# Kernel optimization log

Measured on AMD Instinct MI355X. Metric: run time of the kernel, lower is better.

Reference implementation:

```python
import jax, jax.numpy as jnp
import numpy as np

DIM = 3072
HEADS = 24
HEAD_DIM = 128
MLP_HIDDEN = 12288
SEQ = 2048
BATCH = 1
EPS = 1e-6


def setup_inputs() -> dict:
    key = jax.random.key(0)
    ks = jax.random.split(key, 12)
    s = 0.02
    return {
        "hidden_states": jax.random.normal(ks[0], (BATCH, SEQ, DIM), jnp.float32),
        "temb": jax.random.normal(ks[1], (BATCH, DIM), jnp.float32),
        "rope_cos": jax.random.uniform(ks[2], (SEQ, HEAD_DIM), jnp.float32),
        "rope_sin": jax.random.uniform(ks[3], (SEQ, HEAD_DIM), jnp.float32),
        # AdaLN-Zero single: Linear(dim -> 3*dim)
        "norm_w": jax.random.normal(ks[4], (3 * DIM, DIM), jnp.float32) * s,
        "norm_b": jnp.zeros((3 * DIM,), jnp.float32),
        # fused QKV + MLP projection: Linear(dim -> 3*dim + mlp_hidden)
        "qkv_mlp_w": jax.random.normal(ks[5], (3 * DIM + MLP_HIDDEN, DIM), jnp.float32) * s,
        "qkv_mlp_b": jnp.zeros((3 * DIM + MLP_HIDDEN,), jnp.float32),
        # proj_out: Linear(dim + mlp_hidden -> dim)
        "proj_w": jax.random.normal(ks[6], (DIM, DIM + MLP_HIDDEN), jnp.float32) * s,
        "proj_b": jnp.zeros((DIM,), jnp.float32),
        # qk RMSNorm weights (per head_dim)
        "rms_q_w": jnp.ones((HEAD_DIM,), jnp.float32),
        "rms_k_w": jnp.ones((HEAD_DIM,), jnp.float32),
    }


def _rms_norm(x, w):
    # x: [B,S,H,D], normalize over D
    var = jnp.mean(jnp.square(x), axis=-1, keepdims=True)
    return x * jax.lax.rsqrt(var + EPS) * w


def _apply_rope(x, cos, sin):
    # x: [B,S,H,D]; cos/sin: [S,D]. diffusers use_real, unbind_dim=-1 convention.
    xr = x.reshape(*x.shape[:-1], HEAD_DIM // 2, 2)
    rot = jnp.stack([-xr[..., 1], xr[..., 0]], axis=-1).reshape(x.shape)
    c = cos[None, :, None, :]
    s = sin[None, :, None, :]
    return x * c + rot * s


def reference(hidden_states, temb, rope_cos, rope_sin, norm_w, norm_b,
              qkv_mlp_w, qkv_mlp_b, proj_w, proj_b, rms_q_w, rms_k_w):
    B, S, _ = hidden_states.shape
    residual = hidden_states

    # --- AdaLayerNormZeroSingle ---
    mod = jax.nn.silu(temb) @ norm_w.T + norm_b          # [B, 3*dim]
    shift, scale, gate = jnp.split(mod, 3, axis=-1)       # each [B, dim]
    mu = jnp.mean(hidden_states, axis=-1, keepdims=True)
    var = jnp.mean(jnp.square(hidden_states - mu), axis=-1, keepdims=True)
    ln = (hidden_states - mu) * jax.lax.rsqrt(var + EPS)
    norm_h = ln * (1.0 + scale[:, None, :]) + shift[:, None, :]

    # --- fused QKV + MLP GEMM ---
    qkv_mlp = norm_h @ qkv_mlp_w.T + qkv_mlp_b             # [B,S,3*dim+mlp]
    qkv, mlp_h = jnp.split(qkv_mlp, [3 * DIM], axis=-1)
    mlp_out = jax.nn.gelu(mlp_h, approximate=True)         # tanh GELU

    q, k, v = jnp.split(qkv, 3, axis=-1)
    q = q.reshape(B, S, HEADS, HEAD_DIM)
    k = k.reshape(B, S, HEADS, HEAD_DIM)
    v = v.reshape(B, S, HEADS, HEAD_DIM)

    # qk RMSNorm + RoPE
    q = _apply_rope(_rms_norm(q, rms_q_w), rope_cos, rope_sin)
    k = _apply_rope(_rms_norm(k, rms_k_w), rope_cos, rope_sin)

    # scaled dot-product attention
    scale_f = 1.0 / np.sqrt(HEAD_DIM)
    scores = jnp.einsum("bqhd,bkhd->bhqk", q, k) * scale_f
    probs = jax.nn.softmax(scores, axis=-1)
    attn = jnp.einsum("bhqk,bkhd->bqhd", probs, v).reshape(B, S, DIM)

    # proj_out on concat(attn, gelu(mlp)) + gated residual
    cat = jnp.concatenate([attn, mlp_out], axis=-1)        # [B,S,dim+mlp]
    proj = cat @ proj_w.T + proj_b                          # [B,S,dim]
    return gate[:, None, :] * proj + residual
```

## Files before the change

### kernel.cpp

```cpp
#include <hip/hip_runtime.h>
#include <stdint.h>

typedef __bf16 bf16;
typedef __bf16 bf16x8 __attribute__((ext_vector_type(8)));
typedef __bf16 bf16x4 __attribute__((ext_vector_type(4)));
typedef float f32x4 __attribute__((ext_vector_type(4)));

#define DIM   3072
#define SEQ   2048
#define QKVW  9216
#define MLPH  12288
#define FUSED 21504
#define CATW  15360
#define HD    128
#define NH    24

__device__ __forceinline__ void gload_lds16(const void* g, void* l) {
  __builtin_amdgcn_global_load_lds((__attribute__((address_space(1))) void*)g,
                                   (__attribute__((address_space(3))) void*)l,
                                   16, 0, 0);
}

__global__ __launch_bounds__(256) void k_mod_gemv(
    const float* __restrict__ temb, const float* __restrict__ nw,
    const float* __restrict__ nb, float* __restrict__ mod)
{
  int j = blockIdx.x * 4 + (threadIdx.x >> 6);
  int lane = threadIdx.x & 63;
  const float* row = nw + (size_t)j * DIM;
  float acc = 0.f;
  #pragma unroll
  for (int k0 = 0; k0 < DIM; k0 += 256) {
    int k = k0 + lane * 4;
    float4 w = *(const float4*)(row + k);
    float4 t = *(const float4*)(temb + k);
    float s0 = t.x / (1.f + __expf(-t.x));
    float s1 = t.y / (1.f + __expf(-t.y));
    float s2 = t.z / (1.f + __expf(-t.z));
    float s3 = t.w / (1.f + __expf(-t.w));
    acc += w.x * s0 + w.y * s1 + w.z * s2 + w.w * s3;
  }
  #pragma unroll
  for (int m = 32; m >= 1; m >>= 1) acc += __shfl_xor(acc, m, 64);
  if (lane == 0) mod[j] = acc + nb[j];
}

__global__ __launch_bounds__(256) void k_ln_mod(
    const float* __restrict__ hs, const float* __restrict__ mod,
    bf16* __restrict__ nh)
{
  int m = blockIdx.x;
  int t = threadIdx.x;
  const float* x = hs + (size_t)m * DIM;
  float4 v[3];
  float s = 0.f, ss = 0.f;
  #pragma unroll
  for (int i = 0; i < 3; i++) {
    v[i] = *(const float4*)(x + i * 1024 + t * 4);
    s  += v[i].x + v[i].y + v[i].z + v[i].w;
    ss += v[i].x * v[i].x + v[i].y * v[i].y + v[i].z * v[i].z + v[i].w * v[i].w;
  }
  #pragma unroll
  for (int msk = 32; msk >= 1; msk >>= 1) {
    s  += __shfl_xor(s, msk, 64);
    ss += __shfl_xor(ss, msk, 64);
  }
  __shared__ float red[8];
  int wave = t >> 6;
  if ((t & 63) == 0) { red[wave] = s; red[4 + wave] = ss; }
  __syncthreads();
  s  = red[0] + red[1] + red[2] + red[3];
  ss = red[4] + red[5] + red[6] + red[7];
  float mu  = s * (1.f / DIM);
  float var = ss * (1.f / DIM) - mu * mu;
  float rstd = rsqrtf(var + 1e-6f);
  #pragma unroll
  for (int i = 0; i < 3; i++) {
    int col = i * 1024 + t * 4;
    const float* sc = mod + DIM + col;
    const float* sh = mod + col;
    float4 vv = v[i];
    bf16x4 o;
    o[0] = (bf16)((vv.x - mu) * rstd * (1.f + sc[0]) + sh[0]);
    o[1] = (bf16)((vv.y - mu) * rstd * (1.f + sc[1]) + sh[1]);
    o[2] = (bf16)((vv.z - mu) * rstd * (1.f + sc[2]) + sh[2]);
    o[3] = (bf16)((vv.w - mu) * rstd * (1.f + sc[3]) + sh[3]);
    *(bf16x4*)(nh + (size_t)m * DIM + col) = o;
  }
}

__global__ __launch_bounds__(256) void k_cvt(
    const float* __restrict__ s, bf16* __restrict__ d, size_t n)
{
  size_t stride = (size_t)gridDim.x * 256 * 8;
  for (size_t i = ((size_t)blockIdx.x * 256 + threadIdx.x) * 8; i < n; i += stride) {
    float4 a = *(const float4*)(s + i);
    float4 b = *(const float4*)(s + i + 4);
    bf16x8 h;
    h[0] = (bf16)a.x; h[1] = (bf16)a.y; h[2] = (bf16)a.z; h[3] = (bf16)a.w;
    h[4] = (bf16)b.x; h[5] = (bf16)b.y; h[6] = (bf16)b.z; h[7] = (bf16)b.w;
    *(bf16x8*)(d + i) = h;
  }
}

#define MFMA_B16(a, b, c) __builtin_amdgcn_mfma_f32_16x16x32_bf16(a, b, c, 0, 0, 0)

template<int MODE>
__global__ __launch_bounds__(512, 2) void k_gemm8(
    const bf16* __restrict__ A, const bf16* __restrict__ B,
    const float* __restrict__ bias, int K, int ntn, int nkp,
    bf16* __restrict__ oq, bf16* __restrict__ ocat, float* __restrict__ pk)
{
  __shared__ bf16 lds[65536];
  int tid = threadIdx.x;
  int wave = tid >> 6, lane = tid & 63;
  int wm = wave >> 2, wn = wave & 3;

  int nwg = gridDim.x;
  int bid = blockIdx.x;
  int swz = (bid & 7) * (nwg >> 3) + (bid >> 3);
  int mt = swz & 7;
  int rest = swz >> 3;
  int nt = rest % ntn;
  int kc = rest / ntn;
  int m0 = mt * 256, n0 = nt * 256;
  int Kp = K / nkp;
  int kbeg = kc * Kp;
  int NT = Kp >> 6;

  const bf16* Ag = A + (size_t)m0 * K + kbeg;
  const bf16* Bg = B + (size_t)n0 * K + kbeg;

  auto stA = [&](int kt, int q) {
    int kw = kt >= NT ? kt - NT : kt;
    #pragma unroll
    for (int j = 0; j < 2; j++) {
      int c = j * 16 + q * 8 + wave;
      gload_lds16(Ag + (size_t)((c >> 1) * 16 + (lane & 15)) * K
                     + ((c & 1) * 32 + (lane >> 4) * 8) + kw * 64,
                  &lds[((kt & 1) << 15) + c * 512]);
    }
  };
  auto stB = [&](int kt, int q) {
    int kw = kt >= NT ? kt - NT : kt;
    #pragma unroll
    for (int j = 0; j < 2; j++) {
      int v = j * 8 + wave;
      int c = (v >> 2) * 8 + q * 4 + (v & 3);
      gload_lds16(Bg + (size_t)((c >> 1) * 16 + (lane & 15)) * K
                     + ((c & 1) * 32 + (lane >> 4) * 8) + kw * 64,
                  &lds[((kt & 1) << 15) + 16384 + c * 512]);
    }
  };

  f32x4 acc[8][4];
  #pragma unroll
  for (int i = 0; i < 8; i++)
    #pragma unroll
    for (int j = 0; j < 4; j++) acc[i][j] = (f32x4){0.f, 0.f, 0.f, 0.f};

  const int abase = wm * 8192;
  const int bbase = 16384 + wn * 4096;
  const int lo = lane * 8;
  bf16x8 af[8][2], bfr[4][2];

  #define RD_A(MI0, BO) \
    _Pragma("unroll") for (int mi = 0; mi < 4; mi++) \
    _Pragma("unroll") for (int ks = 0; ks < 2; ks++) \
      af[MI0 + mi][ks] = *(const bf16x8*)&lds[(BO) + abase + ((MI0 + mi) * 2 + ks) * 512 + lo];
  #define RD_B(NI0, BO) \
    _Pragma("unroll") for (int ni = 0; ni < 2; ni++) \
    _Pragma("unroll") for (int ks = 0; ks < 2; ks++) \
      bfr[NI0 + ni][ks] = *(const bf16x8*)&lds[(BO) + bbase + ((NI0 + ni) * 2 + ks) * 512 + lo];
  #define QUAD(MI0, NI0) \
    __builtin_amdgcn_s_setprio(1); \
    _Pragma("unroll") for (int mi = 0; mi < 4; mi++) \
    _Pragma("unroll") for (int ni = 0; ni < 2; ni++) \
    _Pragma("unroll") for (int ks = 0; ks < 2; ks++) \
      acc[MI0 + mi][NI0 + ni] = MFMA_B16(af[MI0 + mi][ks], bfr[NI0 + ni][ks], acc[MI0 + mi][NI0 + ni]); \
    __builtin_amdgcn_s_setprio(0);
  #define BAR()   __builtin_amdgcn_s_barrier()
  #define LGKM0() asm volatile("s_waitcnt lgkmcnt(0)" ::: "memory")
  #define LGKM8() asm volatile("s_waitcnt lgkmcnt(8)" ::: "memory")
  #define VM6()   asm volatile("s_waitcnt vmcnt(6)" ::: "memory")
  #define SB0()   __builtin_amdgcn_sched_barrier(0)

  stA(0, 0); stB(0, 0); stA(0, 1); stB(0, 1);
  stA(1, 0); stB(1, 0); stA(1, 1);
  VM6();
  BAR();

  for (int it = 0; it < NT; it += 2) {
    int ta = it, tb = it + 1;
    RD_A(0, 0) RD_B(0, 0)
    stB(tb, 1);
    LGKM8();
    BAR(); LGKM0(); SB0();
    QUAD(0, 0)
    BAR();
    RD_A(4, 0)
    stA(ta + 2, 0);
    BAR(); LGKM0(); SB0();
    QUAD(4, 0)
    BAR();
    RD_B(2, 0)
    stB(ta + 2, 0);
    BAR(); LGKM0(); SB0();
    QUAD(0, 2)
    BAR();
    stA(ta + 2, 1);
    VM6();
    BAR(); SB0();
    QUAD(4, 2)
    BAR();
    RD_A(0, 32768) RD_B(0, 32768)
    stB(ta + 2, 1);
    LGKM8();
    BAR(); LGKM0(); SB0();
    QUAD(0, 0)
    BAR();
    RD_A(4, 32768)
    stA(tb + 2, 0);
    BAR(); LGKM0(); SB0();
    QUAD(4, 0)
    BAR();
    RD_B(2, 32768)
    stB(tb + 2, 0);
    BAR(); LGKM0(); SB0();
    QUAD(0, 2)
    BAR();
    stA(tb + 2, 1);
    VM6();
    BAR(); SB0();
    QUAD(4, 2)
    BAR();
  }

  int rr = (lane >> 4) * 4, cl = lane & 15;
  int mw0 = m0 + wm * 128, nw0 = n0 + wn * 64;
  #pragma unroll
  for (int mi = 0; mi < 8; mi++) {
    #pragma unroll
    for (int ni = 0; ni < 4; ni++) {
      int n = nw0 + ni * 16 + cl;
      #pragma unroll
      for (int r = 0; r < 4; r++) {
        int m = mw0 + mi * 16 + rr + r;
        float v = acc[mi][ni][r];
        if (MODE == 0) {
          v += bias[n];
          if (n < QKVW) {
            oq[(size_t)m * QKVW + n] = (bf16)v;
          } else {
            float g = 0.5f * v * (1.f + tanhf(0.7978845608028654f * (v + 0.044715f * v * v * v)));
            ocat[(size_t)m * CATW + DIM + (n - QKVW)] = (bf16)g;
          }
        } else {
          pk[(size_t)kc * SEQ * DIM + (size_t)m * DIM + n] = v;
        }
      }
    }
  }
}

template<int MODE>
__global__ __launch_bounds__(256) void k_gemm2(
    const bf16* __restrict__ A, const float* __restrict__ Bf,
    const float* __restrict__ bias, int K, int ntn,
    bf16* __restrict__ oq, bf16* __restrict__ ocat,
    const float* __restrict__ gate, const float* __restrict__ resid,
    float* __restrict__ of)
{
  __shared__ bf16 sA[8192];
  __shared__ bf16 sB[8192];
  int nwg = gridDim.x;
  int bid = blockIdx.x;
  int swz = (bid & 7) * (nwg >> 3) + (bid >> 3);
  int mt = swz & 15, nt = swz >> 4;
  int m0 = mt * 128, n0 = nt * 128;
  int tid = threadIdx.x;
  int wave = tid >> 6, lane = tid & 63;
  int wr = wave >> 1, wc = wave & 1;

  size_t aoff[4], boff[4];
  bf16* la[4];
  bf16* lb[4];
  #pragma unroll
  for (int i = 0; i < 4; i++) {
    int c = wave * 4 + i;
    int rt = c >> 1, kt = c & 1;
    int row = rt * 16 + (lane & 15);
    int col = kt * 32 + (lane >> 4) * 8;
    aoff[i] = (size_t)(m0 + row) * K + col;
    boff[i] = (size_t)(n0 + row) * K + col;
    la[i] = sA + c * 512;
    lb[i] = sB + c * 512;
  }
  f32x4 acc[4][4];
  #pragma unroll
  for (int i = 0; i < 4; i++)
    #pragma unroll
    for (int j = 0; j < 4; j++) acc[i][j] = (f32x4){0.f, 0.f, 0.f, 0.f};

  for (int kk = 0; kk < K; kk += 64) {
    #pragma unroll
    for (int i = 0; i < 4; i++)
      gload_lds16(A + aoff[i] + kk, la[i]);
    #pragma unroll
    for (int i = 0; i < 4; i++) {
      const float* g = Bf + boff[i] + kk;
      float4 f0 = *(const float4*)g;
      float4 f1 = *(const float4*)(g + 4);
      bf16x8 h;
      h[0] = (bf16)f0.x; h[1] = (bf16)f0.y; h[2] = (bf16)f0.z; h[3] = (bf16)f0.w;
      h[4] = (bf16)f1.x; h[5] = (bf16)f1.y; h[6] = (bf16)f1.z; h[7] = (bf16)f1.w;
      *(bf16x8*)(lb[i] + lane * 8) = h;
    }
    __syncthreads();
    #pragma unroll
    for (int ks = 0; ks < 2; ks++) {
      bf16x8 af[4], bfr[4];
      #pragma unroll
      for (int mi = 0; mi < 4; mi++)
        af[mi] = *(const bf16x8*)(sA + ((wr * 4 + mi) * 2 + ks) * 512 + lane * 8);
      #pragma unroll
      for (int nj = 0; nj < 4; nj++)
        bfr[nj] = *(const bf16x8*)(sB + ((wc * 4 + nj) * 2 + ks) * 512 + lane * 8);
      #pragma unroll
      for (int mi = 0; mi < 4; mi++)
        #pragma unroll
        for (int nj = 0; nj < 4; nj++)
          acc[mi][nj] = __builtin_amdgcn_mfma_f32_16x16x32_bf16(af[mi], bfr[nj], acc[mi][nj], 0, 0, 0);
    }
    __syncthreads();
  }

  int rr = (lane >> 4) * 4;
  int cl = lane & 15;
  #pragma unroll
  for (int mi = 0; mi < 4; mi++) {
    #pragma unroll
    for (int nj = 0; nj < 4; nj++) {
      int mbase = m0 + wr * 64 + mi * 16 + rr;
      int n = n0 + wc * 64 + nj * 16 + cl;
      #pragma unroll
      for (int r = 0; r < 4; r++) {
        int m = mbase + r;
        float v = acc[mi][nj][r] + bias[n];
        if (MODE == 0) {
          if (n < QKVW) {
            oq[(size_t)m * QKVW + n] = (bf16)v;
          } else {
            float g = 0.5f * v * (1.f + tanhf(0.7978845608028654f * (v + 0.044715f * v * v * v)));
            ocat[(size_t)m * CATW + DIM + (n - QKVW)] = (bf16)g;
          }
        } else {
          of[(size_t)m * DIM + n] = gate[n] * v + resid[(size_t)m * DIM + n];
        }
      }
    }
  }
}

__global__ __launch_bounds__(256) void k_red(
    const float* __restrict__ pk, const float* __restrict__ bias,
    const float* __restrict__ gate, const float* __restrict__ resid,
    float* __restrict__ out)
{
  int m = blockIdx.x / 3;
  int n = (blockIdx.x % 3) * 1024 + threadIdx.x * 4;
  size_t idx = (size_t)m * DIM + n;
  f32x4 p0 = *(const f32x4*)(pk + idx);
  f32x4 p1 = *(const f32x4*)(pk + (size_t)SEQ * DIM + idx);
  f32x4 b  = *(const f32x4*)(bias + n);
  f32x4 g  = *(const f32x4*)(gate + n);
  f32x4 r  = *(const f32x4*)(resid + idx);
  f32x4 o;
  #pragma unroll
  for (int i = 0; i < 4; i++) o[i] = g[i] * (p0[i] + p1[i] + b[i]) + r[i];
  *(f32x4*)(out + idx) = o;
}

__global__ __launch_bounds__(256) void k_rmsrope(
    bf16* __restrict__ qkv, const float* __restrict__ rc, const float* __restrict__ rs,
    const float* __restrict__ qw, const float* __restrict__ kw)
{
  int srow = blockIdx.x >> 1;
  int isk  = blockIdx.x & 1;
  int off  = isk ? DIM : 0;
  const float* w = isk ? kw : qw;
  int g = threadIdx.x >> 5, gl = threadIdx.x & 31;
  int d = gl * 4;
  #pragma unroll
  for (int hh = 0; hh < 3; hh++) {
    int h = g + hh * 8;
    bf16* p = qkv + (size_t)srow * QKVW + off + h * HD + d;
    bf16x4 u = *(const bf16x4*)p;
    float x0 = (float)u[0], x1 = (float)u[1], x2 = (float)u[2], x3 = (float)u[3];
    float ssq = x0 * x0 + x1 * x1 + x2 * x2 + x3 * x3;
    #pragma unroll
    for (int msk = 16; msk >= 1; msk >>= 1) ssq += __shfl_xor(ssq, msk, 32);
    float r = rsqrtf(ssq * (1.f / HD) + 1e-6f);
    float y0 = x0 * r * w[d], y1 = x1 * r * w[d + 1];
    float y2 = x2 * r * w[d + 2], y3 = x3 * r * w[d + 3];
    const float* c = rc + srow * HD + d;
    const float* sn = rs + srow * HD + d;
    bf16x4 o;
    o[0] = (bf16)(y0 * c[0] - y1 * sn[0]);
    o[1] = (bf16)(y1 * c[1] + y0 * sn[1]);
    o[2] = (bf16)(y2 * c[2] - y3 * sn[2]);
    o[3] = (bf16)(y3 * c[3] + y2 * sn[3]);
    *(bf16x4*)p = o;
  }
}

__global__ __launch_bounds__(256) void k_attn(
    const bf16* __restrict__ qkv, bf16* __restrict__ cat)
{
  int h  = blockIdx.y;
  int q0 = blockIdx.x * 64;
  int tid = threadIdx.x, wave = tid >> 6, lane = tid & 63;
  int r16 = lane & 15, g4 = lane >> 4;
  __shared__ bf16 sK[32 * 136];
  __shared__ bf16 sVt[128 * 40];
  __shared__ bf16 sP[4][16 * 40];

  bf16x8 qf[4];
  {
    int qrow = q0 + wave * 16 + r16;
    const bf16* qp = qkv + (size_t)qrow * QKVW + h * HD + g4 * 8;
    #pragma unroll
    for (int kc = 0; kc < 4; kc++) qf[kc] = *(const bf16x8*)(qp + kc * 32);
  }
  f32x4 oacc[8];
  #pragma unroll
  for (int dc = 0; dc < 8; dc++) oacc[dc] = (f32x4){0.f, 0.f, 0.f, 0.f};
  float mrow[4] = {-1e30f, -1e30f, -1e30f, -1e30f};
  float lrow[4] = {0.f, 0.f, 0.f, 0.f};
  const float scale = 0.08838834764831845f;

  for (int kv0 = 0; kv0 < SEQ; kv0 += 32) {
    {
      int row = tid >> 3, c0 = (tid & 7) * 16;
      const bf16* kp = qkv + (size_t)(kv0 + row) * QKVW + DIM + h * HD + c0;
      uint4 a = *(const uint4*)kp;
      uint4 b = *(const uint4*)(kp + 8);
      *(uint4*)&sK[row * 136 + c0]     = a;
      *(uint4*)&sK[row * 136 + c0 + 8] = b;
    }
    {
      int kv = tid >> 3, c0 = (tid & 7) * 16;
      const bf16* vp = qkv + (size_t)(kv0 + kv) * QKVW + 2 * DIM + h * HD + c0;
      #pragma unroll
      for (int i = 0; i < 4; i++) {
        bf16x4 u = *(const bf16x4*)(vp + i * 4);
        sVt[(c0 + i * 4 + 0) * 40 + kv] = u[0];
        sVt[(c0 + i * 4 + 1) * 40 + kv] = u[1];
        sVt[(c0 + i * 4 + 2) * 40 + kv] = u[2];
        sVt[(c0 + i * 4 + 3) * 40 + kv] = u[3];
      }
    }
    __syncthreads();

    f32x4 sv[2];
    sv[0] = (f32x4){0.f, 0.f, 0.f, 0.f};
    sv[1] = (f32x4){0.f, 0.f, 0.f, 0.f};
    #pragma unroll
    for (int ct = 0; ct < 2; ct++)
      #pragma unroll
      for (int kc = 0; kc < 4; kc++) {
        bf16x8 kf = *(const bf16x8*)&sK[(ct * 16 + r16) * 136 + kc * 32 + g4 * 8];
        sv[ct] = __builtin_amdgcn_mfma_f32_16x16x32_bf16(qf[kc], kf, sv[ct], 0, 0, 0);
      }

    bf16* sPw = &sP[wave][0];
    #pragma unroll
    for (int r = 0; r < 4; r++) {
      float a0 = sv[0][r] * scale, a1 = sv[1][r] * scale;
      float mx = fmaxf(a0, a1);
      #pragma unroll
      for (int msk = 8; msk >= 1; msk >>= 1) mx = fmaxf(mx, __shfl_xor(mx, msk, 16));
      float mnew = fmaxf(mrow[r], mx);
      float so = __expf(mrow[r] - mnew);
      float p0 = __expf(a0 - mnew), p1 = __expf(a1 - mnew);
      float rsum = p0 + p1;
      #pragma unroll
      for (int msk = 8; msk >= 1; msk >>= 1) rsum += __shfl_xor(rsum, msk, 16);
      lrow[r] = lrow[r] * so + rsum;
      mrow[r] = mnew;
      #pragma unroll
      for (int dc = 0; dc < 8; dc++) oacc[dc][r] *= so;
      int prow = g4 * 4 + r;
      sPw[prow * 40 + r16]      = (bf16)p0;
      sPw[prow * 40 + 16 + r16] = (bf16)p1;
    }
    asm volatile("s_waitcnt lgkmcnt(0)" ::: "memory");
    __builtin_amdgcn_sched_barrier(0);
    bf16x8 pa = *(const bf16x8*)&sPw[r16 * 40 + g4 * 8];
    #pragma unroll
    for (int dc = 0; dc < 8; dc++) {
      bf16x8 vf = *(const bf16x8*)&sVt[(dc * 16 + r16) * 40 + g4 * 8];
      oacc[dc] = __builtin_amdgcn_mfma_f32_16x16x32_bf16(pa, vf, oacc[dc], 0, 0, 0);
    }
    __syncthreads();
  }

  #pragma unroll
  for (int dc = 0; dc < 8; dc++) {
    #pragma unroll
    for (int r = 0; r < 4; r++) {
      int qrow = q0 + wave * 16 + g4 * 4 + r;
      int col  = h * HD + dc * 16 + r16;
      cat[(size_t)qrow * CATW + col] = (bf16)(oacc[dc][r] / lrow[r]);
    }
  }
}

extern "C" void kernel_launch(void* const* d_in, const int* in_sizes, int n_in,
                              void* d_out, int out_size, void* d_ws, size_t ws_size,
                              hipStream_t stream) {
  const float* hs      = (const float*)d_in[0];
  const float* temb    = (const float*)d_in[1];
  const float* rope_c  = (const float*)d_in[2];
  const float* rope_s  = (const float*)d_in[3];
  const float* norm_w  = (const float*)d_in[4];
  const float* norm_b  = (const float*)d_in[5];
  const float* qkvml_w = (const float*)d_in[6];
  const float* qkvml_b = (const float*)d_in[7];
  const float* proj_w  = (const float*)d_in[8];
  const float* proj_b  = (const float*)d_in[9];
  const float* rms_q_w = (const float*)d_in[10];
  const float* rms_k_w = (const float*)d_in[11];
  float* out = (float*)d_out;

  char* ws = (char*)d_ws;
  size_t off = 0;
  float* mod  = (float*)(ws + off); off += 40960;
  bf16*  nh   = (bf16*)(ws + off); off += (size_t)SEQ * DIM * 2;
  bf16*  qkvb = (bf16*)(ws + off); off += (size_t)SEQ * QKVW * 2;
  bf16*  catb = (bf16*)(ws + off); off += (size_t)SEQ * CATW * 2;
  bf16*  wqb  = (bf16*)(ws + off); off += (size_t)FUSED * DIM * 2;
  bf16*  wpb  = (bf16*)(ws + off); off += (size_t)DIM * CATW * 2;
  float* pkbf = (float*)(ws + off); off += (size_t)2 * SEQ * DIM * 4;
  bool full = (ws_size >= off);

  if (full) {
    k_cvt<<<dim3(2048), dim3(256), 0, stream>>>(qkvml_w, wqb, (size_t)FUSED * DIM);
    k_cvt<<<dim3(2048), dim3(256), 0, stream>>>(proj_w, wpb, (size_t)DIM * CATW);
  }
  k_mod_gemv<<<dim3(QKVW / 4), dim3(256), 0, stream>>>(temb, norm_w, norm_b, mod);
  k_ln_mod<<<dim3(SEQ), dim3(256), 0, stream>>>(hs, mod, nh);

  if (full) {
    k_gemm8<0><<<dim3(8 * (FUSED / 256)), dim3(512), 0, stream>>>(
        nh, wqb, qkvml_b, DIM, FUSED / 256, 1, qkvb, catb, nullptr);
  } else {
    k_gemm2<0><<<dim3(16 * (FUSED / 128)), dim3(256), 0, stream>>>(
        nh, qkvml_w, qkvml_b, DIM, FUSED / 128, qkvb, catb, nullptr, nullptr, nullptr);
  }

  k_rmsrope<<<dim3(SEQ * 2), dim3(256), 0, stream>>>(qkvb, rope_c, rope_s, rms_q_w, rms_k_w);
  k_attn<<<dim3(SEQ / 64, NH), dim3(256), 0, stream>>>(qkvb, catb);

  if (full) {
    k_gemm8<1><<<dim3(8 * (DIM / 256) * 2), dim3(512), 0, stream>>>(
        catb, wpb, nullptr, CATW, DIM / 256, 2, nullptr, nullptr, pkbf);
    k_red<<<dim3(SEQ * 3), dim3(256), 0, stream>>>(pkbf, proj_b, mod + 2 * DIM, hs, out);
  } else {
    k_gemm2<1><<<dim3(16 * (DIM / 128)), dim3(256), 0, stream>>>(
        catb, proj_w, proj_b, CATW, DIM / 128, nullptr, nullptr, mod + 2 * DIM, hs, out);
  }
}
```

Measured before the change: 1.019 ms.

## Software-pipeline LDS fragment reads in GEMM and prefetch K/V in attention

The GEMM main loop now uses split register sets (aLo/aHi/bLo/bHi) so LDS fragment reads for the next quadrant are issued before the current MFMA quadrant runs. This drops the explicit lgkmcnt waits and sched_barriers, and global-load address offsets are precomputed once. The attention kernel register-prefetches the next K/V tile from global memory while computing on the current one, and pads the K tile row stride to reduce LDS bank conflicts. The cost is higher register pressure, and removing the explicit waits leaves LDS read ordering to the compiler, which may hurt correctness or scheduling.

```diff
diff --git a/kernel.cpp b/kernel.cpp
--- a/kernel.cpp
+++ b/kernel.cpp
@@ -131,26 +131,33 @@
   const bf16* Ag = A + (size_t)m0 * K + kbeg;
   const bf16* Bg = B + (size_t)n0 * K + kbeg;
 
+  int aoffs[2][2], boffs[2][2];
+  int aldc[2][2], bldc[2][2];
+  #pragma unroll
+  for (int q = 0; q < 2; q++) {
+    #pragma unroll
+    for (int j = 0; j < 2; j++) {
+      int ca = j * 16 + q * 8 + wave;
+      aoffs[q][j] = ((ca >> 1) * 16 + (lane & 15)) * K + (ca & 1) * 32 + (lane >> 4) * 8;
+      aldc[q][j] = ca * 512;
+      int v = j * 8 + wave;
+      int cb = (v >> 2) * 8 + q * 4 + (v & 3);
+      boffs[q][j] = ((cb >> 1) * 16 + (lane & 15)) * K + (cb & 1) * 32 + (lane >> 4) * 8;
+      bldc[q][j] = 16384 + cb * 512;
+    }
+  }
+
   auto stA = [&](int kt, int q) {
     int kw = kt >= NT ? kt - NT : kt;
-    #pragma unroll
-    for (int j = 0; j < 2; j++) {
-      int c = j * 16 + q * 8 + wave;
-      gload_lds16(Ag + (size_t)((c >> 1) * 16 + (lane & 15)) * K
-                     + ((c & 1) * 32 + (lane >> 4) * 8) + kw * 64,
-                  &lds[((kt & 1) << 15) + c * 512]);
-    }
+    int bo = (kt & 1) << 15;
+    gload_lds16(Ag + aoffs[q][0] + kw * 64, &lds[bo + aldc[q][0]]);
+    gload_lds16(Ag + aoffs[q][1] + kw * 64, &lds[bo + aldc[q][1]]);
   };
   auto stB = [&](int kt, int q) {
     int kw = kt >= NT ? kt - NT : kt;
-    #pragma unroll
-    for (int j = 0; j < 2; j++) {
-      int v = j * 8 + wave;
-      int c = (v >> 2) * 8 + q * 4 + (v & 3);
-      gload_lds16(Bg + (size_t)((c >> 1) * 16 + (lane & 15)) * K
-                     + ((c & 1) * 32 + (lane >> 4) * 8) + kw * 64,
-                  &lds[((kt & 1) << 15) + 16384 + c * 512]);
-    }
+    int bo = (kt & 1) << 15;
+    gload_lds16(Bg + boffs[q][0] + kw * 64, &lds[bo + bldc[q][0]]);
+    gload_lds16(Bg + boffs[q][1] + kw * 64, &lds[bo + bldc[q][1]]);
   };
 
   f32x4 acc[8][4];
@@ -162,78 +169,74 @@
   const int abase = wm * 8192;
   const int bbase = 16384 + wn * 4096;
   const int lo = lane * 8;
-  bf16x8 af[8][2], bfr[4][2];
-
-  #define RD_A(MI0, BO) \
+  bf16x8 aLo[4][2], aHi[4][2], bLo[2][2], bHi[2][2];
+
+  #define RD_ALO(BO) \
     _Pragma("unroll") for (int mi = 0; mi < 4; mi++) \
     _Pragma("unroll") for (int ks = 0; ks < 2; ks++) \
-      af[MI0 + mi][ks] = *(const bf16x8*)&lds[(BO) + abase + ((MI0 + mi) * 2 + ks) * 512 + lo];
-  #define RD_B(NI0, BO) \
+      aLo[mi][ks] = *(const bf16x8*)&lds[(BO) + abase + (mi * 2 + ks) * 512 + lo];
+  #define RD_AHI(BO) \
+    _Pragma("unroll") for (int mi = 0; mi < 4; mi++) \
+    _Pragma("unroll") for (int ks = 0; ks < 2; ks++) \
+      aHi[mi][ks] = *(const bf16x8*)&lds[(BO) + abase + ((4 + mi) * 2 + ks) * 512 + lo];
+  #define RD_BLO(BO) \
     _Pragma("unroll") for (int ni = 0; ni < 2; ni++) \
     _Pragma("unroll") for (int ks = 0; ks < 2; ks++) \
-      bfr[NI0 + ni][ks] = *(const bf16x8*)&lds[(BO) + bbase + ((NI0 + ni) * 2 + ks) * 512 + lo];
-  #define QUAD(MI0, NI0) \
+      bLo[ni][ks] = *(const bf16x8*)&lds[(BO) + bbase + (ni * 2 + ks) * 512 + lo];
+  #define RD_BHI(BO) \
+    _Pragma("unroll") for (int ni = 0; ni < 2; ni++) \
+    _Pragma("unroll") for (int ks = 0; ks < 2; ks++) \
+      bHi[ni][ks] = *(const bf16x8*)&lds[(BO) + bbase + ((2 + ni) * 2 + ks) * 512 + lo];
+  #define QUAD(AF, BF, MI0, NI0) \
     __builtin_amdgcn_s_setprio(1); \
     _Pragma("unroll") for (int mi = 0; mi < 4; mi++) \
     _Pragma("unroll") for (int ni = 0; ni < 2; ni++) \
     _Pragma("unroll") for (int ks = 0; ks < 2; ks++) \
-      acc[MI0 + mi][NI0 + ni] = MFMA_B16(af[MI0 + mi][ks], bfr[NI0 + ni][ks], acc[MI0 + mi][NI0 + ni]); \
+      acc[MI0 + mi][NI0 + ni] = MFMA_B16(AF[mi][ks], BF[ni][ks], acc[MI0 + mi][NI0 + ni]); \
     __builtin_amdgcn_s_setprio(0);
   #define BAR()   __builtin_amdgcn_s_barrier()
-  #define LGKM0() asm volatile("s_waitcnt lgkmcnt(0)" ::: "memory")
-  #define LGKM8() asm volatile("s_waitcnt lgkmcnt(8)" ::: "memory")
   #define VM6()   asm volatile("s_waitcnt vmcnt(6)" ::: "memory")
-  #define SB0()   __builtin_amdgcn_sched_barrier(0)
 
   stA(0, 0); stB(0, 0); stA(0, 1); stB(0, 1);
   stA(1, 0); stB(1, 0); stA(1, 1);
   VM6();
   BAR();
+  RD_ALO(0) RD_BLO(0)
 
   for (int it = 0; it < NT; it += 2) {
     int ta = it, tb = it + 1;
-    RD_A(0, 0) RD_B(0, 0)
+    BAR();
     stB(tb, 1);
-    LGKM8();
-    BAR(); LGKM0(); SB0();
-    QUAD(0, 0)
-    BAR();
-    RD_A(4, 0)
+    RD_AHI(0)
+    QUAD(aLo, bLo, 0, 0)
+    BAR();
     stA(ta + 2, 0);
-    BAR(); LGKM0(); SB0();
-    QUAD(4, 0)
-    BAR();
-    RD_B(2, 0)
+    RD_BHI(0)
+    QUAD(aHi, bLo, 4, 0)
+    BAR();
     stB(ta + 2, 0);
-    BAR(); LGKM0(); SB0();
-    QUAD(0, 2)
-    BAR();
+    QUAD(aLo, bHi, 0, 2)
     stA(ta + 2, 1);
     VM6();
-    BAR(); SB0();
-    QUAD(4, 2)
-    BAR();
-    RD_A(0, 32768) RD_B(0, 32768)
+    BAR();
+    RD_ALO(32768) RD_BLO(32768)
+    QUAD(aHi, bHi, 4, 2)
+    BAR();
     stB(ta + 2, 1);
-    LGKM8();
-    BAR(); LGKM0(); SB0();
-    QUAD(0, 0)
-    BAR();
-    RD_A(4, 32768)
+    RD_AHI(32768)
+    QUAD(aLo, bLo, 0, 0)
+    BAR();
     stA(tb + 2, 0);
-    BAR(); LGKM0(); SB0();
-    QUAD(4, 0)
-    BAR();
-    RD_B(2, 32768)
+    RD_BHI(32768)
+    QUAD(aHi, bLo, 4, 0)
+    BAR();
     stB(tb + 2, 0);
-    BAR(); LGKM0(); SB0();
-    QUAD(0, 2)
-    BAR();
+    QUAD(aLo, bHi, 0, 2)
     stA(tb + 2, 1);
     VM6();
-    BAR(); SB0();
-    QUAD(4, 2)
-    BAR();
+    BAR();
+    RD_ALO(0) RD_BLO(0)
+    QUAD(aHi, bHi, 4, 2)
   }
 
   int rr = (lane >> 4) * 4, cl = lane & 15;
@@ -261,6 +264,13 @@
       }
     }
   }
+  #undef RD_ALO
+  #undef RD_AHI
+  #undef RD_BLO
+  #undef RD_BHI
+  #undef QUAD
+  #undef BAR
+  #undef VM6
 }
 
 template<int MODE>
@@ -421,7 +431,7 @@
   int q0 = blockIdx.x * 64;
   int tid = threadIdx.x, wave = tid >> 6, lane = tid & 63;
   int r16 = lane & 15, g4 = lane >> 4;
-  __shared__ bf16 sK[32 * 136];
+  __shared__ bf16 sK[32 * 168];
   __shared__ bf16 sVt[128 * 40];
   __shared__ bf16 sP[4][16 * 40];
 
@@ -439,28 +449,32 @@
   float lrow[4] = {0.f, 0.f, 0.f, 0.f};
   const float scale = 0.08838834764831845f;
 
+  int krow = tid >> 3, c0 = (tid & 7) * 16;
+  const bf16* kbase = qkv + (size_t)krow * QKVW + DIM + h * HD + c0;
+  const bf16* vbase = qkv + (size_t)krow * QKVW + 2 * DIM + h * HD + c0;
+
+  bf16x8 kr0 = *(const bf16x8*)(kbase);
+  bf16x8 kr1 = *(const bf16x8*)(kbase + 8);
+  bf16x8 vr0 = *(const bf16x8*)(vbase);
+  bf16x8 vr1 = *(const bf16x8*)(vbase + 8);
+
   for (int kv0 = 0; kv0 < SEQ; kv0 += 32) {
-    {
-      int row = tid >> 3, c0 = (tid & 7) * 16;
-      const bf16* kp = qkv + (size_t)(kv0 + row) * QKVW + DIM + h * HD + c0;
-      uint4 a = *(const uint4*)kp;
-      uint4 b = *(const uint4*)(kp + 8);
-      *(uint4*)&sK[row * 136 + c0]     = a;
-      *(uint4*)&sK[row * 136 + c0 + 8] = b;
-    }
-    {
-      int kv = tid >> 3, c0 = (tid & 7) * 16;
-      const bf16* vp = qkv + (size_t)(kv0 + kv) * QKVW + 2 * DIM + h * HD + c0;
-      #pragma unroll
-      for (int i = 0; i < 4; i++) {
-        bf16x4 u = *(const bf16x4*)(vp + i * 4);
-        sVt[(c0 + i * 4 + 0) * 40 + kv] = u[0];
-        sVt[(c0 + i * 4 + 1) * 40 + kv] = u[1];
-        sVt[(c0 + i * 4 + 2) * 40 + kv] = u[2];
-        sVt[(c0 + i * 4 + 3) * 40 + kv] = u[3];
-      }
+    *(bf16x8*)&sK[krow * 168 + c0]     = kr0;
+    *(bf16x8*)&sK[krow * 168 + c0 + 8] = kr1;
+    #pragma unroll
+    for (int i = 0; i < 8; i++) {
+      sVt[(c0 + i) * 40 + krow]     = vr0[i];
+      sVt[(c0 + 8 + i) * 40 + krow] = vr1[i];
     }
     __syncthreads();
+    if (kv0 + 32 < SEQ) {
+      const bf16* kn = kbase + (size_t)(kv0 + 32) * QKVW;
+      const bf16* vn = vbase + (size_t)(kv0 + 32) * QKVW;
+      kr0 = *(const bf16x8*)(kn);
+      kr1 = *(const bf16x8*)(kn + 8);
+      vr0 = *(const bf16x8*)(vn);
+      vr1 = *(const bf16x8*)(vn + 8);
+    }
 
     f32x4 sv[2];
     sv[0] = (f32x4){0.f, 0.f, 0.f, 0.f};
@@ -469,7 +483,7 @@
     for (int ct = 0; ct < 2; ct++)
       #pragma unroll
       for (int kc = 0; kc < 4; kc++) {
-        bf16x8 kf = *(const bf16x8*)&sK[(ct * 16 + r16) * 136 + kc * 32 + g4 * 8];
+        bf16x8 kf = *(const bf16x8*)&sK[(ct * 16 + r16) * 168 + kc * 32 + g4 * 8];
         sv[ct] = __builtin_amdgcn_mfma_f32_16x16x32_bf16(qf[kc], kf, sv[ct], 0, 0, 0);
       }
 
```

Measured after the change: 1.069 ms. +4.9%, slower.
